# Optimization experiments

Hardware: AMD Instinct MI355X
Metric: run time of the kernel (lower is better)

## Reference

```python
import jax, jax.numpy as jnp
import numpy as np
from math import sqrt

W_SIZE = jnp.array([32, 64, 128, 256, 32, 64, 128, 256], dtype=jnp.int32)  # per-head window

def setup_inputs() -> dict:
    key = jax.random.key(0)
    kq, kk, kv = jax.random.split(key, 3)
    B, L, H, E = 4, 2048, 8, 64
    D = 64
    return {
        "queries": jax.random.normal(kq, (B, L, H, E), dtype=jnp.float32),
        "keys": jax.random.normal(kk, (B, L, H, E), dtype=jnp.float32),
        "values": jax.random.normal(kv, (B, L, H, D), dtype=jnp.float32),
    }

def reference(queries, keys, values):
    B, L, H, E = queries.shape
    scale = 1.0 / sqrt(E)
    # dense scores: [B, H, L, L]
    scores = jnp.einsum('blhe,bshe->bhls', queries, keys)
    # per-head band mask: |i - j| <= w[h]  -> [H, L, L]
    i = jnp.arange(L)
    diff = jnp.abs(i[:, None] - i[None, :])            # [L, L]
    band = diff[None, :, :] <= W_SIZE[:, None, None]   # [H, L, L]
    scores = jnp.where(band[None], scores, -jnp.inf)
    A = jax.nn.softmax(scale * scores, axis=-1)        # dropout p=0 (eval)
    V = jnp.einsum('bhls,bshd->blhd', A, values)
    return V
```

## Files before the change

kernel.cpp:

```cpp
#include <hip/hip_runtime.h>
#include <math.h>


#define LL 2048
#define HH 8
#define EE 64
#define DD 64
#define RS (HH * EE)

typedef __attribute__((ext_vector_type(8))) short short8;
typedef __attribute__((ext_vector_type(4))) float floatx4;
typedef __attribute__((ext_vector_type(4))) _Float16 half4;
typedef __attribute__((ext_vector_type(2))) __fp16 fp16x2;

static __device__ __forceinline__ unsigned f2bf(float f) {
    union { float f; unsigned u; } v; v.f = f;
    return (v.u + 0x7fff + ((v.u >> 16) & 1)) >> 16;
}
static __device__ __forceinline__ unsigned pack2(float a, float b) {
    return f2bf(a) | (f2bf(b) << 16);
}
static __device__ __forceinline__ unsigned packh2(float a, float b) {
    union { fp16x2 h; unsigned u; } v;
    v.h = __builtin_amdgcn_cvt_pkrtz(a, b);
    return v.u;
}

static __device__ __forceinline__ void barrier_nodrain() {
    asm volatile("s_waitcnt lgkmcnt(0)" ::: "memory");
    __builtin_amdgcn_s_barrier();
}

#define K_BUF(cu)  (sAll + (cu) * 4096)
#define V_BUF(cu)  (sAll + 8192 + (cu) * 4608)

static __device__ __forceinline__ void compute_tile(
    int j0, const short* __restrict__ kbase, const short* __restrict__ vbase,
    int w, int qb, int iq, int quad, int l15,
    short8 qf0, short8 qf1, floatx4* __restrict__ acc, float& lsum)
{
#pragma unroll
    for (int t4 = 0; t4 < 4; ++t4) {
        const int jb = j0 + t4 * 16;
        if (jb > qb + 15 + w || jb + 15 < qb - w) continue;
        const bool needMask = ((jb + 15 - qb) > w) || ((qb + 15 - jb) > w);

        const short* kp = kbase + 1024 * t4 + 128 * quad + 8 * l15;
        short8 k0 = *(const short8*)kp;
        short8 k1 = *(const short8*)(kp + 512);
        floatx4 st = {};
        st = __builtin_amdgcn_mfma_f32_16x16x32_bf16(k0, qf0, st, 0, 0, 0);
        st = __builtin_amdgcn_mfma_f32_16x16x32_bf16(k1, qf1, st, 0, 0, 0);

        float pr[4];
        const int jq = jb + quad * 4;
#pragma unroll
        for (int r = 0; r < 4; ++r) {
            float x = st[r];
            if (needMask) {
                const int di = iq - (jq + r);
                x = (di <= w && di >= -w) ? x : -INFINITY;
            }
            pr[r] = __expf(x);
            lsum += pr[r];
        }
        half4 pf;
        {
            union { half4 v; unsigned u[2]; } pu;
            pu.u[0] = packh2(pr[0], pr[1]);
            pu.u[1] = packh2(pr[2], pr[3]);
            pf = pu.v;
        }
#pragma unroll
        for (int nt = 0; nt < 4; ++nt) {
            half4 vf = *(const half4*)(vbase + (nt * 16 + l15) * 72 + t4 * 16 + quad * 4);
            acc[nt] = __builtin_amdgcn_mfma_f32_16x16x16f16(pf, vf, acc[nt], 0, 0, 0);
        }
    }
}

#define ISSUE(jn, kf0_, kf1_, vv_)                                              \
    {                                                                           \
        const float4* src_ = (const float4*)(Kb + (size_t)((jn) + rowp) * RS + cp); \
        kf0_ = src_[0]; kf1_ = src_[1];                                         \
        _Pragma("unroll")                                                       \
        for (int rr_ = 0; rr_ < 8; ++rr_)                                       \
            vv_[rr_] = Vb[(size_t)((jn) + wv * 8 + rr_) * RS + lane];           \
    }

#define STAGE(bufIdx, kf0_, kf1_, vv_)                                          \
    {                                                                           \
        uint4 u0_ = { pack2(kf0_.x,kf0_.y), pack2(kf0_.z,kf0_.w),               \
                      pack2(kf1_.x,kf1_.y), pack2(kf1_.z,kf1_.w) };             \
        *(uint4*)&K_BUF(bufIdx)[kWoff] = u0_;                                   \
        uint4 w0_ = { packh2(vv_[0],vv_[1]), packh2(vv_[2],vv_[3]),             \
                      packh2(vv_[4],vv_[5]), packh2(vv_[6],vv_[7]) };           \
        *(uint4*)&V_BUF(bufIdx)[vWoff] = w0_;                                   \
    }

__global__ __launch_bounds__(512, 4) void mwa_r11(
    const float* __restrict__ Q,
    const float* __restrict__ K,
    const float* __restrict__ V,
    float* __restrict__ O)
{
    const int tid  = threadIdx.x;
    const int lane = tid & 63;
    const int wv   = tid >> 6;
    const int quad = lane >> 4;
    const int l15  = lane & 15;

    const int gid   = blockIdx.x;
    const int heavy = (gid >> 8) == 0;
    const int c     = gid & 255;
    const int it    = c >> 4;
    const int rem   = c & 15;
    const int b     = rem >> 2;
    const int z     = rem & 3;
    const int hb    = z >> 1;
    const int p     = z & 1;
    const int h     = hb * 4 + (heavy ? (3 - p) : p);
    const int i0    = it << 7;
    const int w     = 32 << (h & 3);

    alignas(16) __shared__ short sAll[17408];

    const float* Qb = Q + ((size_t)b * LL * HH + h) * EE;
    const float* Kb = K + ((size_t)b * LL * HH + h) * EE;
    const float* Vb = V + ((size_t)b * LL * HH + h) * DD;
    float*       Ob = O + ((size_t)b * LL * HH + h) * DD;

    {
        const float sc = 0.125f;
        const int row = tid >> 2, cc = (tid & 3) << 4;
        const float4* src = (const float4*)(Qb + (size_t)(i0 + row) * RS + cc);
        float4 f0 = src[0], f1 = src[1], f2 = src[2], f3 = src[3];
        uint4 u0 = { pack2(sc*f0.x,sc*f0.y), pack2(sc*f0.z,sc*f0.w),
                     pack2(sc*f1.x,sc*f1.y), pack2(sc*f1.z,sc*f1.w) };
        uint4 u1 = { pack2(sc*f2.x,sc*f2.y), pack2(sc*f2.z,sc*f2.w),
                     pack2(sc*f3.x,sc*f3.y), pack2(sc*f3.z,sc*f3.w) };
        uint4* dst = (uint4*)&sAll[row * 72 + cc];
        dst[0] = u0; dst[1] = u1;
    }
    __syncthreads();
    short8 qf0, qf1;
    {
        const short* qp = &sAll[(wv * 16 + l15) * 72 + quad * 8];
        qf0 = *(const short8*)qp;
        qf1 = *(const short8*)(qp + 32);
    }
    __syncthreads();

    const int jt_lo = max(0, i0 - w) >> 6;
    const int jt_hi = min(LL - 1, i0 + 127 + w) >> 6;
    const int n     = jt_hi - jt_lo + 1;

    const int rowp  = tid >> 3, cp = (tid & 7) << 3;
    const int jtw   = rowp >> 4, l15w = rowp & 15, ks = cp >> 5, q0w = (cp >> 3) & 3;
    const int kWoff = (((jtw * 2 + ks) * 4 + q0w) * 16 + l15w) * 8;
    const int vWoff = lane * 72 + wv * 8;

    float4 kA0, kA1; float vA[8];
    float4 kB0, kB1; float vB[8];
    ISSUE(jt_lo << 6, kA0, kA1, vA);
    STAGE(0, kA0, kA1, vA);
    if (n > 1) ISSUE((jt_lo + 1) << 6, kA0, kA1, vA);
    __syncthreads();

    floatx4 acc[4] = {};
    float lsum = 0.f;
    const int iq = i0 + wv * 16 + l15;
    const int qb = i0 + wv * 16;

    for (int s = 0; s < n; s += 2) {
        const int jt = jt_lo + s;
        if (s + 2 < n) ISSUE((jt + 2) << 6, kB0, kB1, vB);
        if (s + 1 < n) STAGE(1, kA0, kA1, vA);
        compute_tile(jt << 6, K_BUF(0), V_BUF(0), w, qb, iq, quad, l15, qf0, qf1, acc, lsum);
        barrier_nodrain();

        if (s + 1 < n) {
            if (s + 3 < n) ISSUE((jt + 3) << 6, kA0, kA1, vA);
            if (s + 2 < n) STAGE(0, kB0, kB1, vB);
            compute_tile((jt + 1) << 6, K_BUF(1), V_BUF(1), w, qb, iq, quad, l15, qf0, qf1, acc, lsum);
            barrier_nodrain();
        }
    }

    lsum += __shfl_xor(lsum, 16, 64);
    lsum += __shfl_xor(lsum, 32, 64);
    float rinv[4];
#pragma unroll
    for (int r = 0; r < 4; ++r) {
        const float lr = __shfl(lsum, quad * 4 + r, 64);
        rinv[r] = 1.0f / lr;
    }
#pragma unroll
    for (int nt = 0; nt < 4; ++nt) {
#pragma unroll
        for (int r = 0; r < 4; ++r) {
            Ob[(size_t)(i0 + wv * 16 + quad * 4 + r) * RS + nt * 16 + l15]
                = acc[nt][r] * rinv[r];
        }
    }
}

extern "C" void kernel_launch(void* const* d_in, const int* in_sizes, int n_in,
                              void* d_out, int out_size, void* d_ws, size_t ws_size,
                              hipStream_t stream)
{
    const float* Q = (const float*)d_in[0];
    const float* K = (const float*)d_in[1];
    const float* V = (const float*)d_in[2];
    float* O = (float*)d_out;

    dim3 grid(512), block(512);
    hipLaunchKernelGGL(mwa_r11, grid, block, 0, stream, Q, K, V, O);
}
```

Before: 101.5 us.

## Pre-convert K/V to packed bf16/fp16 tiles in a prep kernel

Adds a prep kernel that converts K to bf16 and V to transposed fp16 once, writing them into the workspace in the exact shared-memory tile layout. The main kernel then fills each tile with one contiguous 16-byte load and store per thread, replacing the strided fp32 loads and per-tile packing. Because attention windows overlap, this removes repeated conversion of the same K/V tiles and halves the bytes fetched per tile. The cost is an extra kernel launch plus a workspace write and read. The old path remains as a fallback when the workspace is too small.

```diff
diff --git a/kernel.cpp b/kernel.cpp
--- a/kernel.cpp
+++ b/kernel.cpp
@@ -79,29 +79,60 @@
     }
 }
 
-#define ISSUE(jn, kf0_, kf1_, vv_)                                              \
-    {                                                                           \
-        const float4* src_ = (const float4*)(Kb + (size_t)((jn) + rowp) * RS + cp); \
-        kf0_ = src_[0]; kf1_ = src_[1];                                         \
-        _Pragma("unroll")                                                       \
-        for (int rr_ = 0; rr_ < 8; ++rr_)                                       \
-            vv_[rr_] = Vb[(size_t)((jn) + wv * 8 + rr_) * RS + lane];           \
-    }
-
-#define STAGE(bufIdx, kf0_, kf1_, vv_)                                          \
-    {                                                                           \
-        uint4 u0_ = { pack2(kf0_.x,kf0_.y), pack2(kf0_.z,kf0_.w),               \
-                      pack2(kf1_.x,kf1_.y), pack2(kf1_.z,kf1_.w) };             \
-        *(uint4*)&K_BUF(bufIdx)[kWoff] = u0_;                                   \
-        uint4 w0_ = { packh2(vv_[0],vv_[1]), packh2(vv_[2],vv_[3]),             \
-                      packh2(vv_[4],vv_[5]), packh2(vv_[6],vv_[7]) };           \
-        *(uint4*)&V_BUF(bufIdx)[vWoff] = w0_;                                   \
-    }
-
-__global__ __launch_bounds__(512, 4) void mwa_r11(
+__global__ __launch_bounds__(256, 8) void mwa_prep(
+    const float* __restrict__ K, const float* __restrict__ V,
+    short* __restrict__ wsK, short* __restrict__ wsV)
+{
+    const int t   = blockIdx.x;
+    const int jt  = t & 31;
+    const int h   = (t >> 5) & 7;
+    const int b   = t >> 8;
+    const int j0  = jt << 6;
+    const int tid = threadIdx.x;
+
+    const float* Kt = K + ((size_t)(b * LL + j0) * HH + h) * EE;
+    const float* Vt = V + ((size_t)(b * LL + j0) * HH + h) * DD;
+    short* wk = wsK + (size_t)((b * HH + h) * 32 + jt) * 4096;
+    short* wv = wsV + (size_t)((b * HH + h) * 32 + jt) * 4096;
+
+    __shared__ float sV[64 * 68];
+
+#pragma unroll
+    for (int uu = 0; uu < 2; ++uu) {
+        const int u = tid + uu * 256;
+        const int row = u >> 3, cg = u & 7;
+        const float4* src = (const float4*)(Kt + (size_t)row * RS + cg * 8);
+        float4 f0 = src[0], f1 = src[1];
+        uint4 o = { pack2(f0.x,f0.y), pack2(f0.z,f0.w),
+                    pack2(f1.x,f1.y), pack2(f1.z,f1.w) };
+        *(uint4*)&wk[((((row >> 4) * 2 + (cg >> 2)) * 4 + (cg & 3)) * 16 + (row & 15)) * 8] = o;
+    }
+
+    {
+        const int row = tid >> 2, dg = (tid & 3) << 4;
+        const float4* src = (const float4*)(Vt + (size_t)row * RS + dg);
+        float4 f0 = src[0], f1 = src[1], f2 = src[2], f3 = src[3];
+        *(float4*)&sV[row * 68 + dg     ] = f0;
+        *(float4*)&sV[row * 68 + dg + 4 ] = f1;
+        *(float4*)&sV[row * 68 + dg + 8 ] = f2;
+        *(float4*)&sV[row * 68 + dg + 12] = f3;
+    }
+    __syncthreads();
+    {
+        const int d = tid >> 2, jp = (tid & 3) << 4;
+        unsigned o[8];
+#pragma unroll
+        for (int r = 0; r < 8; ++r)
+            o[r] = packh2(sV[(jp + 2 * r) * 68 + d], sV[(jp + 2 * r + 1) * 68 + d]);
+        *(uint4*)&wv[d * 64 + jp    ] = *(uint4*)&o[0];
+        *(uint4*)&wv[d * 64 + jp + 8] = *(uint4*)&o[4];
+    }
+}
+
+__global__ __launch_bounds__(512, 4) void mwa_r12(
     const float* __restrict__ Q,
-    const float* __restrict__ K,
-    const float* __restrict__ V,
+    const short* __restrict__ wsK,
+    const short* __restrict__ wsV,
     float* __restrict__ O)
 {
     const int tid  = threadIdx.x;
@@ -125,10 +156,10 @@
 
     alignas(16) __shared__ short sAll[17408];
 
-    const float* Qb = Q + ((size_t)b * LL * HH + h) * EE;
-    const float* Kb = K + ((size_t)b * LL * HH + h) * EE;
-    const float* Vb = V + ((size_t)b * LL * HH + h) * DD;
-    float*       Ob = O + ((size_t)b * LL * HH + h) * DD;
+    const float* Qb  = Q + ((size_t)b * LL * HH + h) * EE;
+    const short* wKt = wsK + (size_t)((b * HH + h) * 32) * 4096;
+    const short* wVt = wsV + (size_t)((b * HH + h) * 32) * 4096;
+    float*       Ob  = O + ((size_t)b * LL * HH + h) * DD;
 
     {
         const float sc = 0.125f;
@@ -155,6 +186,140 @@
     const int jt_hi = min(LL - 1, i0 + 127 + w) >> 6;
     const int n     = jt_hi - jt_lo + 1;
 
+    const int vOff = (tid >> 3) * 72 + (tid & 7) * 8;
+
+#define ISSUE(jti_, kr_, vr_)                                        \
+    {                                                                \
+        kr_ = *(const uint4*)&wKt[(size_t)(jti_) * 4096 + tid * 8];  \
+        vr_ = *(const uint4*)&wVt[(size_t)(jti_) * 4096 + tid * 8];  \
+    }
+#define STAGE(bufIdx, kr_, vr_)                                      \
+    {                                                                \
+        *(uint4*)&K_BUF(bufIdx)[tid * 8] = kr_;                      \
+        *(uint4*)&V_BUF(bufIdx)[vOff]    = vr_;                      \
+    }
+
+    uint4 kA, vA, kB, vB;
+    ISSUE(jt_lo, kA, vA);
+    STAGE(0, kA, vA);
+    if (n > 1) ISSUE(jt_lo + 1, kA, vA);
+    __syncthreads();
+
+    floatx4 acc[4] = {};
+    float lsum = 0.f;
+    const int iq = i0 + wv * 16 + l15;
+    const int qb = i0 + wv * 16;
+
+    for (int s = 0; s < n; s += 2) {
+        const int jt = jt_lo + s;
+        if (s + 2 < n) ISSUE(jt + 2, kB, vB);
+        if (s + 1 < n) STAGE(1, kA, vA);
+        compute_tile(jt << 6, K_BUF(0), V_BUF(0), w, qb, iq, quad, l15, qf0, qf1, acc, lsum);
+        barrier_nodrain();
+
+        if (s + 1 < n) {
+            if (s + 3 < n) ISSUE(jt + 3, kA, vA);
+            if (s + 2 < n) STAGE(0, kB, vB);
+            compute_tile((jt + 1) << 6, K_BUF(1), V_BUF(1), w, qb, iq, quad, l15, qf0, qf1, acc, lsum);
+            barrier_nodrain();
+        }
+    }
+#undef ISSUE
+#undef STAGE
+
+    lsum += __shfl_xor(lsum, 16, 64);
+    lsum += __shfl_xor(lsum, 32, 64);
+    float rinv[4];
+#pragma unroll
+    for (int r = 0; r < 4; ++r) {
+        const float lr = __shfl(lsum, quad * 4 + r, 64);
+        rinv[r] = 1.0f / lr;
+    }
+#pragma unroll
+    for (int nt = 0; nt < 4; ++nt) {
+#pragma unroll
+        for (int r = 0; r < 4; ++r) {
+            Ob[(size_t)(i0 + wv * 16 + quad * 4 + r) * RS + nt * 16 + l15]
+                = acc[nt][r] * rinv[r];
+        }
+    }
+}
+
+#define ISSUE_F(jn, kf0_, kf1_, vv_)                                            \
+    {                                                                           \
+        const float4* src_ = (const float4*)(Kb + (size_t)((jn) + rowp) * RS + cp); \
+        kf0_ = src_[0]; kf1_ = src_[1];                                         \
+        _Pragma("unroll")                                                       \
+        for (int rr_ = 0; rr_ < 8; ++rr_)                                       \
+            vv_[rr_] = Vb[(size_t)((jn) + wv * 8 + rr_) * RS + lane];           \
+    }
+#define STAGE_F(bufIdx, kf0_, kf1_, vv_)                                        \
+    {                                                                           \
+        uint4 u0_ = { pack2(kf0_.x,kf0_.y), pack2(kf0_.z,kf0_.w),               \
+                      pack2(kf1_.x,kf1_.y), pack2(kf1_.z,kf1_.w) };             \
+        *(uint4*)&K_BUF(bufIdx)[kWoff] = u0_;                                   \
+        uint4 w0_ = { packh2(vv_[0],vv_[1]), packh2(vv_[2],vv_[3]),             \
+                      packh2(vv_[4],vv_[5]), packh2(vv_[6],vv_[7]) };           \
+        *(uint4*)&V_BUF(bufIdx)[vWoff] = w0_;                                   \
+    }
+
+__global__ __launch_bounds__(512, 4) void mwa_r11f(
+    const float* __restrict__ Q,
+    const float* __restrict__ K,
+    const float* __restrict__ V,
+    float* __restrict__ O)
+{
+    const int tid  = threadIdx.x;
+    const int lane = tid & 63;
+    const int wv   = tid >> 6;
+    const int quad = lane >> 4;
+    const int l15  = lane & 15;
+
+    const int gid   = blockIdx.x;
+    const int heavy = (gid >> 8) == 0;
+    const int c     = gid & 255;
+    const int it    = c >> 4;
+    const int rem   = c & 15;
+    const int b     = rem >> 2;
+    const int z     = rem & 3;
+    const int hb    = z >> 1;
+    const int p     = z & 1;
+    const int h     = hb * 4 + (heavy ? (3 - p) : p);
+    const int i0    = it << 7;
+    const int w     = 32 << (h & 3);
+
+    alignas(16) __shared__ short sAll[17408];
+
+    const float* Qb = Q + ((size_t)b * LL * HH + h) * EE;
+    const float* Kb = K + ((size_t)b * LL * HH + h) * EE;
+    const float* Vb = V + ((size_t)b * LL * HH + h) * DD;
+    float*       Ob = O + ((size_t)b * LL * HH + h) * DD;
+
+    {
+        const float sc = 0.125f;
+        const int row = tid >> 2, cc = (tid & 3) << 4;
+        const float4* src = (const float4*)(Qb + (size_t)(i0 + row) * RS + cc);
+        float4 f0 = src[0], f1 = src[1], f2 = src[2], f3 = src[3];
+        uint4 u0 = { pack2(sc*f0.x,sc*f0.y), pack2(sc*f0.z,sc*f0.w),
+                     pack2(sc*f1.x,sc*f1.y), pack2(sc*f1.z,sc*f1.w) };
+        uint4 u1 = { pack2(sc*f2.x,sc*f2.y), pack2(sc*f2.z,sc*f2.w),
+                     pack2(sc*f3.x,sc*f3.y), pack2(sc*f3.z,sc*f3.w) };
+        uint4* dst = (uint4*)&sAll[row * 72 + cc];
+        dst[0] = u0; dst[1] = u1;
+    }
+    __syncthreads();
+    short8 qf0, qf1;
+    {
+        const short* qp = &sAll[(wv * 16 + l15) * 72 + quad * 8];
+        qf0 = *(const short8*)qp;
+        qf1 = *(const short8*)(qp + 32);
+    }
+    __syncthreads();
+
+    const int jt_lo = max(0, i0 - w) >> 6;
+    const int jt_hi = min(LL - 1, i0 + 127 + w) >> 6;
+    const int n     = jt_hi - jt_lo + 1;
+
     const int rowp  = tid >> 3, cp = (tid & 7) << 3;
     const int jtw   = rowp >> 4, l15w = rowp & 15, ks = cp >> 5, q0w = (cp >> 3) & 3;
     const int kWoff = (((jtw * 2 + ks) * 4 + q0w) * 16 + l15w) * 8;
@@ -162,9 +327,9 @@
 
     float4 kA0, kA1; float vA[8];
     float4 kB0, kB1; float vB[8];
-    ISSUE(jt_lo << 6, kA0, kA1, vA);
-    STAGE(0, kA0, kA1, vA);
-    if (n > 1) ISSUE((jt_lo + 1) << 6, kA0, kA1, vA);
+    ISSUE_F(jt_lo << 6, kA0, kA1, vA);
+    STAGE_F(0, kA0, kA1, vA);
+    if (n > 1) ISSUE_F((jt_lo + 1) << 6, kA0, kA1, vA);
     __syncthreads();
 
     floatx4 acc[4] = {};
@@ -174,14 +339,14 @@
 
     for (int s = 0; s < n; s += 2) {
         const int jt = jt_lo + s;
-        if (s + 2 < n) ISSUE((jt + 2) << 6, kB0, kB1, vB);
-        if (s + 1 < n) STAGE(1, kA0, kA1, vA);
+        if (s + 2 < n) ISSUE_F((jt + 2) << 6, kB0, kB1, vB);
+        if (s + 1 < n) STAGE_F(1, kA0, kA1, vA);
         compute_tile(jt << 6, K_BUF(0), V_BUF(0), w, qb, iq, quad, l15, qf0, qf1, acc, lsum);
         barrier_nodrain();
 
         if (s + 1 < n) {
-            if (s + 3 < n) ISSUE((jt + 3) << 6, kA0, kA1, vA);
-            if (s + 2 < n) STAGE(0, kB0, kB1, vB);
+            if (s + 3 < n) ISSUE_F((jt + 3) << 6, kA0, kA1, vA);
+            if (s + 2 < n) STAGE_F(0, kB0, kB1, vB);
             compute_tile((jt + 1) << 6, K_BUF(1), V_BUF(1), w, qb, iq, quad, l15, qf0, qf1, acc, lsum);
             barrier_nodrain();
         }
@@ -214,6 +379,13 @@
     const float* V = (const float*)d_in[2];
     float* O = (float*)d_out;
 
-    dim3 grid(512), block(512);
-    hipLaunchKernelGGL(mwa_r11, grid, block, 0, stream, Q, K, V, O);
-}
+    const size_t wsNeed = (size_t)2 * 4 * 8 * 32 * 4096 * sizeof(short);
+    if (ws_size >= wsNeed) {
+        short* wsK = (short*)d_ws;
+        short* wsV = wsK + (size_t)4 * 8 * 32 * 4096;
+        hipLaunchKernelGGL(mwa_prep, dim3(1024), dim3(256), 0, stream, K, V, wsK, wsV);
+        hipLaunchKernelGGL(mwa_r12, dim3(512), dim3(512), 0, stream, Q, wsK, wsV, O);
+    } else {
+        hipLaunchKernelGGL(mwa_r11f, dim3(512), dim3(512), 0, stream, Q, K, V, O);
+    }
+}
```

Result: slower. 109.4 us (+7.8%).
